# Performance work log

Hardware: AMD Instinct MI355X
Metric: run time of the kernel (lower is better)

Reference implementation:

```python
import jax, jax.numpy as jnp
import numpy as np

EMBED_DIM = 1024
NUM_HEADS = 16
HEAD_DIM = EMBED_DIM // NUM_HEADS


def setup_inputs() -> dict:
    key = jax.random.key(0)
    k_x, k_wqkv, k_bqkv, k_wp, k_bp = jax.random.split(key, 5)
    B, S = 4, 2048
    scale = 1.0 / np.sqrt(EMBED_DIM)
    return {
        "x": jax.random.normal(k_x, (B, S, EMBED_DIM), dtype=jnp.float32),
        "w_qkv": jax.random.uniform(k_wqkv, (EMBED_DIM, 3 * EMBED_DIM), jnp.float32, -scale, scale),
        "b_qkv": jax.random.uniform(k_bqkv, (3 * EMBED_DIM,), jnp.float32, -scale, scale),
        "w_proj": jax.random.uniform(k_wp, (EMBED_DIM, EMBED_DIM), jnp.float32, -scale, scale),
        "b_proj": jax.random.uniform(k_bp, (EMBED_DIM,), jnp.float32, -scale, scale),
    }


def reference(x, w_qkv, b_qkv, w_proj, b_proj):
    B, S, E = x.shape
    H, D = NUM_HEADS, HEAD_DIM
    # fused QKV projection: [B,S,3E] -> [3,B,H,S,D]
    qkv = (x @ w_qkv + b_qkv).reshape(B, S, 3, H, D).transpose(2, 0, 3, 1, 4)
    q, k, v = qkv[0], qkv[1], qkv[2]
    scores = jnp.einsum("bhqd,bhkd->bhqk", q, k) / np.sqrt(D).astype(jnp.float32)
    attn = jax.nn.softmax(scores, axis=-1)  # dropout is identity in eval
    out = jnp.einsum("bhqk,bhkd->bhqd", attn, v)
    out = out.transpose(0, 2, 1, 3).reshape(B, S, E)
    return out @ w_proj + b_proj
```

## Files before the change

kernel.cpp:

```cpp
#include <hip/hip_runtime.h>
#include <hip/hip_bf16.h>

#define PB 4
#define PS 2048
#define PH 16
#define PD 64
#define PE 1024

typedef short v8s __attribute__((ext_vector_type(8)));
typedef float v4f __attribute__((ext_vector_type(4)));

__device__ __forceinline__ ushort f2b(float f) {
  union { __hip_bfloat16 b; ushort u; } cv;
  cv.b = __float2bfloat16(f);
  return cv.u;
}

__device__ __forceinline__ void cp16(const __hip_bfloat16* g, __hip_bfloat16* l) {
  __builtin_amdgcn_global_load_lds(
      (const __attribute__((address_space(1))) void*)g,
      (__attribute__((address_space(3))) void*)l, 16, 0, 0);
}

__global__ __launch_bounds__(256) void conv_f2b(const float* __restrict__ S,
                                                __hip_bfloat16* __restrict__ D) {
  int i = blockIdx.x * 256 + threadIdx.x;
  float4 f = reinterpret_cast<const float4*>(S)[i];
  union { ushort u[4]; uint2 v; } pk;
  pk.u[0] = f2b(f.x); pk.u[1] = f2b(f.y); pk.u[2] = f2b(f.z); pk.u[3] = f2b(f.w);
  reinterpret_cast<uint2*>(D)[i] = pk.v;
}

__global__ __launch_bounds__(256) void transp_f2b(const float* __restrict__ S,
                                                  __hip_bfloat16* __restrict__ D,
                                                  int R, int C) {
  __shared__ float tile[32][33];
  const int t = threadIdx.x;
  const int tx = t & 31, ty = t >> 5;
  const int r0 = blockIdx.y * 32, c0 = blockIdx.x * 32;
#pragma unroll
  for (int i = 0; i < 4; ++i)
    tile[ty + 8 * i][tx] = S[(size_t)(r0 + ty + 8 * i) * C + c0 + tx];
  __syncthreads();
#pragma unroll
  for (int i = 0; i < 4; ++i)
    D[(size_t)(c0 + ty + 8 * i) * R + r0 + tx] = __float2bfloat16(tile[tx][ty + 8 * i]);
}

template <int MODE>
__global__ __launch_bounds__(256) void gemm_bt(
    const __hip_bfloat16* __restrict__ A, const __hip_bfloat16* __restrict__ BT,
    const float* __restrict__ bias, void* __restrict__ outv) {
  __shared__ __hip_bfloat16 As[128 * 64];
  __shared__ __hip_bfloat16 Bs[128 * 64];
  const int t = threadIdx.x;
  const int lane = t & 63, w = t >> 6;
  const int ln = lane & 15, qd = lane >> 4;
  const int wm = w >> 1, wn = w & 1;
  const int m0 = blockIdx.y * 128, n0 = blockIdx.x * 128;
  v4f acc[4][4] = {};

  for (int k0 = 0; k0 < PE; k0 += 64) {
    __syncthreads();
#pragma unroll
    for (int i = 0; i < 4; ++i) {
      int idx = t + 256 * i;
      int r = idx >> 3, cs = idx & 7;
      int cg = cs ^ (r & 7);
      cp16(A + (size_t)(m0 + r) * PE + k0 + cg * 8, As + idx * 8);
      cp16(BT + (size_t)(n0 + r) * PE + k0 + cg * 8, Bs + idx * 8);
    }
    __syncthreads();
#pragma unroll
    for (int kk = 0; kk < 2; ++kk) {
      v8s af[4], bf[4];
#pragma unroll
      for (int mb = 0; mb < 4; ++mb) {
        int ra = wm * 64 + mb * 16 + ln;
        int ca = (kk * 4 + qd) ^ (ra & 7);
        af[mb] = *reinterpret_cast<const v8s*>(As + ra * 64 + ca * 8);
      }
#pragma unroll
      for (int nb = 0; nb < 4; ++nb) {
        int rb = wn * 64 + nb * 16 + ln;
        int cb = (kk * 4 + qd) ^ (rb & 7);
        bf[nb] = *reinterpret_cast<const v8s*>(Bs + rb * 64 + cb * 8);
      }
#pragma unroll
      for (int mb = 0; mb < 4; ++mb)
#pragma unroll
        for (int nb = 0; nb < 4; ++nb)
          acc[mb][nb] = __builtin_amdgcn_mfma_f32_16x16x32_bf16(af[mb], bf[nb],
                                                                acc[mb][nb], 0, 0, 0);
    }
  }

  const int mwb = m0 + wm * 64 + qd * 4;
  const int nwb = n0 + wn * 64 + ln;
  if (MODE == 0) {
    __hip_bfloat16* QKV = (__hip_bfloat16*)outv;
#pragma unroll
    for (int nb = 0; nb < 4; ++nb) {
      int n = nwb + nb * 16;
      float bv = bias[n];
      int which = n >> 10, h = (n >> 6) & 15, d = n & 63;
#pragma unroll
      for (int mb = 0; mb < 4; ++mb) {
        int r0 = mwb + mb * 16;
        int b = r0 >> 11, s0 = r0 & (PS - 1);
        v4f a = acc[mb][nb];
        if (which == 2) {
          union { ushort u[4]; uint2 v; } pk;
#pragma unroll
          for (int i = 0; i < 4; ++i) pk.u[i] = f2b(a[i] + bv);
          size_t idx = (((size_t)(2 * PB + b) * PH + h) * PD + d) * PS + s0;
          *reinterpret_cast<uint2*>(&QKV[idx]) = pk.v;
        } else {
          float sc = (which == 0) ? 0.125f : 1.0f;
          size_t base = (((size_t)(which * PB + b) * PH + h) * PS + s0) * PD + d;
#pragma unroll
          for (int i = 0; i < 4; ++i)
            QKV[base + (size_t)i * PD] = __float2bfloat16((a[i] + bv) * sc);
        }
      }
    }
  } else {
    float* Co = (float*)outv;
#pragma unroll
    for (int nb = 0; nb < 4; ++nb) {
      int n = nwb + nb * 16;
      float bv = bias[n];
#pragma unroll
      for (int mb = 0; mb < 4; ++mb) {
        int r0 = mwb + mb * 16;
        v4f a = acc[mb][nb];
#pragma unroll
        for (int i = 0; i < 4; ++i)
          Co[(size_t)(r0 + i) * PE + n] = a[i] + bv;
      }
    }
  }
}

__global__ __launch_bounds__(256) void attn_mfma3(
    const __hip_bfloat16* __restrict__ QKV, __hip_bfloat16* __restrict__ O) {
  __shared__ __hip_bfloat16 Ks[128 * 64];
  __shared__ __hip_bfloat16 Vts[64 * 128];
  __shared__ __hip_bfloat16 Ps[128][136];
  const int t = threadIdx.x;
  const int lane = t & 63, w = t >> 6;
  const int ln = lane & 15, qd = lane >> 4;
  const int b = blockIdx.y >> 4, h = blockIdx.y & 15;
  const int q0 = blockIdx.x * 128;
  const __hip_bfloat16* Qb = QKV + (size_t)(b * PH + h) * PS * PD;
  const __hip_bfloat16* Kb = QKV + (size_t)((PB + b) * PH + h) * PS * PD;
  const __hip_bfloat16* Vb = QKV + (size_t)((2 * PB + b) * PH + h) * PD * PS;

  v8s qf[2][2];
#pragma unroll
  for (int u = 0; u < 2; ++u) {
    size_t qr = (size_t)(q0 + 32 * w + 16 * u + ln) * PD;
    qf[u][0] = *reinterpret_cast<const v8s*>(Qb + qr + qd * 8);
    qf[u][1] = *reinterpret_cast<const v8s*>(Qb + qr + 32 + qd * 8);
  }
  v4f oacc[2][4] = {};
  float lrow[2] = {0.f, 0.f};

  for (int kt = 0; kt < PS; kt += 128) {
    __syncthreads();
#pragma unroll
    for (int i = 0; i < 4; ++i) {
      int idx = t + 256 * i;
      int rk = idx >> 3, ck = (idx & 7) ^ (rk & 7);
      cp16(Kb + (size_t)(kt + rk) * PD + ck * 8, Ks + idx * 8);
      int rv = idx >> 4, cv = (idx & 15) ^ (rv & 7);
      cp16(Vb + (size_t)rv * PS + kt + cv * 8, Vts + idx * 8);
    }
    __syncthreads();

#pragma unroll
    for (int u = 0; u < 2; ++u) {
      float psum = 0.f;
#pragma unroll
      for (int nb = 0; nb < 8; ++nb) {
        int nr = nb * 16 + ln;
        int c0 = qd ^ (nr & 7);
        v8s k0 = *reinterpret_cast<const v8s*>(Ks + nr * 64 + c0 * 8);
        v8s k1 = *reinterpret_cast<const v8s*>(Ks + nr * 64 + (c0 ^ 4) * 8);
        v4f z = {};
        z = __builtin_amdgcn_mfma_f32_16x16x32_bf16(k0, qf[u][0], z, 0, 0, 0);
        v4f sv = __builtin_amdgcn_mfma_f32_16x16x32_bf16(k1, qf[u][1], z, 0, 0, 0);
        union { ushort pu[4]; uint2 pv; } pk;
#pragma unroll
        for (int i = 0; i < 4; ++i) {
          float p = __expf(sv[i]);
          psum += p;
          pk.pu[i] = f2b(p);
        }
        *reinterpret_cast<uint2*>(&Ps[32 * w + 16 * u + ln][nb * 16 + qd * 4]) = pk.pv;
      }
      psum += __shfl_xor(psum, 16);
      psum += __shfl_xor(psum, 32);
      lrow[u] += psum;
    }
    v8s pf[2][4];
#pragma unroll
    for (int u = 0; u < 2; ++u)
#pragma unroll
      for (int s = 0; s < 4; ++s)
        pf[u][s] = *reinterpret_cast<const v8s*>(
            &Ps[32 * w + 16 * u + ln][s * 32 + qd * 8]);
#pragma unroll
    for (int db = 0; db < 4; ++db) {
      int rv = db * 16 + ln;
      v4f o0 = oacc[0][db], o1 = oacc[1][db];
#pragma unroll
      for (int s = 0; s < 4; ++s) {
        int cv = (s * 4 + qd) ^ (rv & 7);
        v8s vf = *reinterpret_cast<const v8s*>(Vts + rv * 128 + cv * 8);
        o0 = __builtin_amdgcn_mfma_f32_16x16x32_bf16(pf[0][s], vf, o0, 0, 0, 0);
        o1 = __builtin_amdgcn_mfma_f32_16x16x32_bf16(pf[1][s], vf, o1, 0, 0, 0);
      }
      oacc[0][db] = o0;
      oacc[1][db] = o1;
    }
  }
#pragma unroll
  for (int u = 0; u < 2; ++u) {
#pragma unroll
    for (int i = 0; i < 4; ++i) {
      float inv = 1.f / __shfl(lrow[u], qd * 4 + i);
      int sg = q0 + 32 * w + 16 * u + qd * 4 + i;
      size_t base = (((size_t)b * PS + sg) * PH + h) * PD;
#pragma unroll
      for (int db = 0; db < 4; ++db)
        O[base + db * 16 + ln] = __float2bfloat16(oacc[u][db][i] * inv);
    }
  }
}

__device__ __forceinline__ uint2 load4bf(const float* p) {
  const float4 f = *reinterpret_cast<const float4*>(p);
  union { ushort u[4]; uint2 v; } pk;
  pk.u[0] = f2b(f.x); pk.u[1] = f2b(f.y); pk.u[2] = f2b(f.z); pk.u[3] = f2b(f.w);
  return pk.v;
}
__device__ __forceinline__ uint2 load4bf(const __hip_bfloat16* p) {
  return *reinterpret_cast<const uint2*>(p);
}

template <typename AT, int MODE>
__global__ __launch_bounds__(256) void gemm128(
    const AT* __restrict__ A, const float* __restrict__ Bm,
    const float* __restrict__ bias, void* __restrict__ outv, int ldb) {
  __shared__ __hip_bfloat16 As[128][40];
  __shared__ __hip_bfloat16 Bs[128][40];
  const int t = threadIdx.x;
  const int lane = t & 63, w = t >> 6;
  const int ln = lane & 15, qd = lane >> 4;
  const int wm = w >> 1, wn = w & 1;
  const int m0 = blockIdx.y * 128, n0 = blockIdx.x * 128;
  v4f acc[4][4] = {};
  for (int k0 = 0; k0 < PE; k0 += 32) {
    __syncthreads();
#pragma unroll
    for (int i = 0; i < 4; ++i) {
      int p = t + 256 * i;
      int m = p >> 3, kc = p & 7;
      *reinterpret_cast<uint2*>(&As[m][kc * 4]) =
          load4bf(A + (size_t)(m0 + m) * PE + k0 + kc * 4);
    }
#pragma unroll
    for (int i = 0; i < 4; ++i) {
      int p = t + 256 * i;
      int n = p & 127, kc = p >> 7;
      union { ushort u[4]; uint2 v; } pk;
#pragma unroll
      for (int r = 0; r < 4; ++r)
        pk.u[r] = f2b(Bm[(size_t)(k0 + kc * 4 + r) * ldb + n0 + n]);
      *reinterpret_cast<uint2*>(&Bs[n][kc * 4]) = pk.v;
    }
    __syncthreads();
    v8s af[4], bf[4];
#pragma unroll
    for (int mb = 0; mb < 4; ++mb)
      af[mb] = *reinterpret_cast<const v8s*>(&As[wm * 64 + mb * 16 + ln][qd * 8]);
#pragma unroll
    for (int nb = 0; nb < 4; ++nb)
      bf[nb] = *reinterpret_cast<const v8s*>(&Bs[wn * 64 + nb * 16 + ln][qd * 8]);
#pragma unroll
    for (int mb = 0; mb < 4; ++mb)
#pragma unroll
      for (int nb = 0; nb < 4; ++nb)
        acc[mb][nb] = __builtin_amdgcn_mfma_f32_16x16x32_bf16(af[mb], bf[nb],
                                                              acc[mb][nb], 0, 0, 0);
  }
  const int mwb = m0 + wm * 64 + qd * 4;
  const int nwb = n0 + wn * 64 + ln;
  if (MODE == 0) {
    __hip_bfloat16* QKV = (__hip_bfloat16*)outv;
#pragma unroll
    for (int nb = 0; nb < 4; ++nb) {
      int n = nwb + nb * 16;
      float bv = bias[n];
      int which = n >> 10, h = (n >> 6) & 15, d = n & 63;
#pragma unroll
      for (int mb = 0; mb < 4; ++mb) {
        int r0 = mwb + mb * 16;
        int b = r0 >> 11, s0 = r0 & (PS - 1);
        v4f a = acc[mb][nb];
        if (which == 2) {
          union { ushort u[4]; uint2 v; } pk;
#pragma unroll
          for (int i = 0; i < 4; ++i) pk.u[i] = f2b(a[i] + bv);
          size_t idx = (((size_t)(2 * PB + b) * PH + h) * PD + d) * PS + s0;
          *reinterpret_cast<uint2*>(&QKV[idx]) = pk.v;
        } else {
          float sc = (which == 0) ? 0.125f : 1.0f;
          size_t base = (((size_t)(which * PB + b) * PH + h) * PS + s0) * PD + d;
#pragma unroll
          for (int i = 0; i < 4; ++i)
            QKV[base + (size_t)i * PD] = __float2bfloat16((a[i] + bv) * sc);
        }
      }
    }
  } else {
    float* Co = (float*)outv;
#pragma unroll
    for (int nb = 0; nb < 4; ++nb) {
      int n = nwb + nb * 16;
      float bv = bias[n];
#pragma unroll
      for (int mb = 0; mb < 4; ++mb) {
        int r0 = mwb + mb * 16;
        v4f a = acc[mb][nb];
#pragma unroll
        for (int i = 0; i < 4; ++i)
          Co[(size_t)(r0 + i) * PE + n] = a[i] + bv;
      }
    }
  }
}

extern "C" void kernel_launch(void* const* d_in, const int* in_sizes, int n_in,
                              void* d_out, int out_size, void* d_ws,
                              size_t ws_size, hipStream_t stream) {
  const float* x = (const float*)d_in[0];
  const float* w_qkv = (const float*)d_in[1];
  const float* b_qkv = (const float*)d_in[2];
  const float* w_proj = (const float*)d_in[3];
  const float* b_proj = (const float*)d_in[4];
  float* out = (float*)d_out;

  const size_t xE = (size_t)PB * PS * PE;
  const size_t wqE = (size_t)PE * 3 * PE;
  const size_t wpE = (size_t)PE * PE;
  const size_t qkvE = (size_t)3 * PB * PH * PS * PD;
  const size_t needMain = (xE + wqE + wpE + qkvE) * 2;

  dim3 blk(256);
  dim3 gq(24, 64), ga(16, 64), gp(8, 64);

  if (ws_size >= needMain) {
    __hip_bfloat16* xb = (__hip_bfloat16*)d_ws;
    __hip_bfloat16* wqkvT = xb + xE;
    __hip_bfloat16* wprojT = wqkvT + wqE;
    __hip_bfloat16* qkv = wprojT + wpE;
    __hip_bfloat16* o = xb;

    conv_f2b<<<dim3(xE / 1024), blk, 0, stream>>>(x, xb);
    transp_f2b<<<dim3(96, 32), blk, 0, stream>>>(w_qkv, wqkvT, PE, 3 * PE);
    transp_f2b<<<dim3(32, 32), blk, 0, stream>>>(w_proj, wprojT, PE, PE);
    gemm_bt<0><<<gq, blk, 0, stream>>>(xb, wqkvT, b_qkv, qkv);
    attn_mfma3<<<ga, blk, 0, stream>>>(qkv, o);
    gemm_bt<1><<<gp, blk, 0, stream>>>(o, wprojT, b_proj, out);
  } else {
    __hip_bfloat16* qkv = (__hip_bfloat16*)d_ws;
    if (ws_size >= (qkvE + xE) * 2) {
      __hip_bfloat16* o = qkv + qkvE;
      gemm128<float, 0><<<gq, blk, 0, stream>>>(x, w_qkv, b_qkv, qkv, 3 * PE);
      attn_mfma3<<<ga, blk, 0, stream>>>(qkv, o);
      gemm128<__hip_bfloat16, 1><<<gp, blk, 0, stream>>>(o, w_proj, b_proj, out, PE);
    } else {
      __hip_bfloat16* o = (__hip_bfloat16*)d_out;
      float* tmp = (float*)d_ws;
      gemm128<float, 0><<<gq, blk, 0, stream>>>(x, w_qkv, b_qkv, qkv, 3 * PE);
      attn_mfma3<<<ga, blk, 0, stream>>>(qkv, o);
      gemm128<__hip_bfloat16, 1><<<gp, blk, 0, stream>>>(o, w_proj, b_proj, tmp, PE);
      hipMemcpyAsync(d_out, tmp, xE * sizeof(float), hipMemcpyDeviceToDevice, stream);
    }
  }
}
```

Before: 310.3 us.

## Enlarge GEMM tile to 256x128 and hoist K fragments in attention

The bf16 GEMM block tile grows from 128x128 to 256x128. Each of the four waves now owns a 64x128 sub-tile with 32 accumulators, which halves the grid in M and raises arithmetic intensity per shared-memory load of B. In the attention kernel, K fragments are loaded from LDS once per tile into registers and reused by both query sub-blocks, instead of being reloaded per sub-block. Both changes raise register pressure, which may reduce occupancy or cause spills. The larger LDS footprint for A and the smaller grid (768 and 256 blocks) could hurt latency hiding.

```diff
diff --git a/kernel.cpp b/kernel.cpp
--- a/kernel.cpp
+++ b/kernel.cpp
@@ -51,56 +51,61 @@
 __global__ __launch_bounds__(256) void gemm_bt(
     const __hip_bfloat16* __restrict__ A, const __hip_bfloat16* __restrict__ BT,
     const float* __restrict__ bias, void* __restrict__ outv) {
-  __shared__ __hip_bfloat16 As[128 * 64];
+  __shared__ __hip_bfloat16 As[256 * 64];
   __shared__ __hip_bfloat16 Bs[128 * 64];
   const int t = threadIdx.x;
   const int lane = t & 63, w = t >> 6;
   const int ln = lane & 15, qd = lane >> 4;
-  const int wm = w >> 1, wn = w & 1;
-  const int m0 = blockIdx.y * 128, n0 = blockIdx.x * 128;
-  v4f acc[4][4] = {};
+  const int m0 = blockIdx.y * 256, n0 = blockIdx.x * 128;
+  v4f acc[4][8] = {};
 
   for (int k0 = 0; k0 < PE; k0 += 64) {
     __syncthreads();
+#pragma unroll
+    for (int i = 0; i < 8; ++i) {
+      int idx = t + 256 * i;
+      int r = idx >> 3, cs = idx & 7;
+      int cg = cs ^ (r & 7);
+      cp16(A + (size_t)(m0 + r) * PE + k0 + cg * 8, As + idx * 8);
+    }
 #pragma unroll
     for (int i = 0; i < 4; ++i) {
       int idx = t + 256 * i;
       int r = idx >> 3, cs = idx & 7;
       int cg = cs ^ (r & 7);
-      cp16(A + (size_t)(m0 + r) * PE + k0 + cg * 8, As + idx * 8);
       cp16(BT + (size_t)(n0 + r) * PE + k0 + cg * 8, Bs + idx * 8);
     }
     __syncthreads();
 #pragma unroll
     for (int kk = 0; kk < 2; ++kk) {
-      v8s af[4], bf[4];
+      v8s af[4], bf[8];
 #pragma unroll
       for (int mb = 0; mb < 4; ++mb) {
-        int ra = wm * 64 + mb * 16 + ln;
+        int ra = w * 64 + mb * 16 + ln;
         int ca = (kk * 4 + qd) ^ (ra & 7);
         af[mb] = *reinterpret_cast<const v8s*>(As + ra * 64 + ca * 8);
       }
 #pragma unroll
-      for (int nb = 0; nb < 4; ++nb) {
-        int rb = wn * 64 + nb * 16 + ln;
+      for (int nb = 0; nb < 8; ++nb) {
+        int rb = nb * 16 + ln;
         int cb = (kk * 4 + qd) ^ (rb & 7);
         bf[nb] = *reinterpret_cast<const v8s*>(Bs + rb * 64 + cb * 8);
       }
 #pragma unroll
       for (int mb = 0; mb < 4; ++mb)
 #pragma unroll
-        for (int nb = 0; nb < 4; ++nb)
+        for (int nb = 0; nb < 8; ++nb)
           acc[mb][nb] = __builtin_amdgcn_mfma_f32_16x16x32_bf16(af[mb], bf[nb],
                                                                 acc[mb][nb], 0, 0, 0);
     }
   }
 
-  const int mwb = m0 + wm * 64 + qd * 4;
-  const int nwb = n0 + wn * 64 + ln;
+  const int mwb = m0 + w * 64 + qd * 4;
+  const int nwb = n0 + ln;
   if (MODE == 0) {
     __hip_bfloat16* QKV = (__hip_bfloat16*)outv;
 #pragma unroll
-    for (int nb = 0; nb < 4; ++nb) {
+    for (int nb = 0; nb < 8; ++nb) {
       int n = nwb + nb * 16;
       float bv = bias[n];
       int which = n >> 10, h = (n >> 6) & 15, d = n & 63;
@@ -127,7 +132,7 @@
   } else {
     float* Co = (float*)outv;
 #pragma unroll
-    for (int nb = 0; nb < 4; ++nb) {
+    for (int nb = 0; nb < 8; ++nb) {
       int n = nwb + nb * 16;
       float bv = bias[n];
 #pragma unroll
@@ -178,18 +183,22 @@
     }
     __syncthreads();
 
+    v8s kf[8][2];
+#pragma unroll
+    for (int nb = 0; nb < 8; ++nb) {
+      int nr = nb * 16 + ln;
+      int c0 = qd ^ (nr & 7);
+      kf[nb][0] = *reinterpret_cast<const v8s*>(Ks + nr * 64 + c0 * 8);
+      kf[nb][1] = *reinterpret_cast<const v8s*>(Ks + nr * 64 + (c0 ^ 4) * 8);
+    }
 #pragma unroll
     for (int u = 0; u < 2; ++u) {
       float psum = 0.f;
 #pragma unroll
       for (int nb = 0; nb < 8; ++nb) {
-        int nr = nb * 16 + ln;
-        int c0 = qd ^ (nr & 7);
-        v8s k0 = *reinterpret_cast<const v8s*>(Ks + nr * 64 + c0 * 8);
-        v8s k1 = *reinterpret_cast<const v8s*>(Ks + nr * 64 + (c0 ^ 4) * 8);
         v4f z = {};
-        z = __builtin_amdgcn_mfma_f32_16x16x32_bf16(k0, qf[u][0], z, 0, 0, 0);
-        v4f sv = __builtin_amdgcn_mfma_f32_16x16x32_bf16(k1, qf[u][1], z, 0, 0, 0);
+        z = __builtin_amdgcn_mfma_f32_16x16x32_bf16(kf[nb][0], qf[u][0], z, 0, 0, 0);
+        v4f sv = __builtin_amdgcn_mfma_f32_16x16x32_bf16(kf[nb][1], qf[u][1], z, 0, 0, 0);
         union { ushort pu[4]; uint2 pv; } pk;
 #pragma unroll
         for (int i = 0; i < 4; ++i) {
@@ -359,7 +368,7 @@
   const size_t needMain = (xE + wqE + wpE + qkvE) * 2;
 
   dim3 blk(256);
-  dim3 gq(24, 64), ga(16, 64), gp(8, 64);
+  dim3 gq(24, 32), ga(16, 64), gp(8, 32);
 
   if (ws_size >= needMain) {
     __hip_bfloat16* xb = (__hip_bfloat16*)d_ws;
@@ -376,17 +385,18 @@
     gemm_bt<1><<<gp, blk, 0, stream>>>(o, wprojT, b_proj, out);
   } else {
     __hip_bfloat16* qkv = (__hip_bfloat16*)d_ws;
+    dim3 gq128(24, 64), gp128(8, 64);
     if (ws_size >= (qkvE + xE) * 2) {
       __hip_bfloat16* o = qkv + qkvE;
-      gemm128<float, 0><<<gq, blk, 0, stream>>>(x, w_qkv, b_qkv, qkv, 3 * PE);
+      gemm128<float, 0><<<gq128, blk, 0, stream>>>(x, w_qkv, b_qkv, qkv, 3 * PE);
       attn_mfma3<<<ga, blk, 0, stream>>>(qkv, o);
-      gemm128<__hip_bfloat16, 1><<<gp, blk, 0, stream>>>(o, w_proj, b_proj, out, PE);
+      gemm128<__hip_bfloat16, 1><<<gp128, blk, 0, stream>>>(o, w_proj, b_proj, out, PE);
     } else {
       __hip_bfloat16* o = (__hip_bfloat16*)d_out;
       float* tmp = (float*)d_ws;
-      gemm128<float, 0><<<gq, blk, 0, stream>>>(x, w_qkv, b_qkv, qkv, 3 * PE);
+      gemm128<float, 0><<<gq128, blk, 0, stream>>>(x, w_qkv, b_qkv, qkv, 3 * PE);
       attn_mfma3<<<ga, blk, 0, stream>>>(qkv, o);
-      gemm128<__hip_bfloat16, 1><<<gp, blk, 0, stream>>>(o, w_proj, b_proj, tmp, PE);
+      gemm128<__hip_bfloat16, 1><<<gp128, blk, 0, stream>>>(o, w_proj, b_proj, tmp, PE);
       hipMemcpyAsync(d_out, tmp, xE * sizeof(float), hipMemcpyDeviceToDevice, stream);
     }
   }
```

After: 338.6 us. 1.09x slower.

## Read V directly from global, per-wave swizzled P buffer, exp2 softmax

Applied to the files above, without the earlier changes.

The attention kernel stops staging V tiles in shared memory and reads V fragments straight from global memory (through cache). It also replaces the shared 128x136 P buffer with per-wave swizzled 16x128 buffers, and hoists the K fragment loads out of the u-loop into registers. Q is prescaled by log2(e)/8 so exp2f can replace __expf. These changes aim to cut LDS traffic, shared-memory footprint and the exp cost, at the price of uncoalesced global V reads and higher register pressure. The softmax still has no max subtraction, which was already the case before.

```diff
diff --git a/kernel.cpp b/kernel.cpp
--- a/kernel.cpp
+++ b/kernel.cpp
@@ -1,11 +1,14 @@
 #include <hip/hip_runtime.h>
 #include <hip/hip_bf16.h>
+#include <math.h>
 
 #define PB 4
 #define PS 2048
 #define PH 16
 #define PD 64
 #define PE 1024
+
+#define QSCALE 0.1803368801111244f
 
 typedef short v8s __attribute__((ext_vector_type(8)));
 typedef float v4f __attribute__((ext_vector_type(4)));
@@ -116,7 +119,7 @@
           size_t idx = (((size_t)(2 * PB + b) * PH + h) * PD + d) * PS + s0;
           *reinterpret_cast<uint2*>(&QKV[idx]) = pk.v;
         } else {
-          float sc = (which == 0) ? 0.125f : 1.0f;
+          float sc = (which == 0) ? QSCALE : 1.0f;
           size_t base = (((size_t)(which * PB + b) * PH + h) * PS + s0) * PD + d;
 #pragma unroll
           for (int i = 0; i < 4; ++i)
@@ -142,11 +145,10 @@
   }
 }
 
-__global__ __launch_bounds__(256) void attn_mfma3(
+__global__ __launch_bounds__(256) void attn_mfma4(
     const __hip_bfloat16* __restrict__ QKV, __hip_bfloat16* __restrict__ O) {
   __shared__ __hip_bfloat16 Ks[128 * 64];
-  __shared__ __hip_bfloat16 Vts[64 * 128];
-  __shared__ __hip_bfloat16 Ps[128][136];
+  __shared__ __hip_bfloat16 Psr[4][16 * 128];
   const int t = threadIdx.x;
   const int lane = t & 63, w = t >> 6;
   const int ln = lane & 15, qd = lane >> 4;
@@ -155,6 +157,7 @@
   const __hip_bfloat16* Qb = QKV + (size_t)(b * PH + h) * PS * PD;
   const __hip_bfloat16* Kb = QKV + (size_t)((PB + b) * PH + h) * PS * PD;
   const __hip_bfloat16* Vb = QKV + (size_t)((2 * PB + b) * PH + h) * PD * PS;
+  __hip_bfloat16* myP = &Psr[w][0];
 
   v8s qf[2][2];
 #pragma unroll
@@ -173,51 +176,52 @@
       int idx = t + 256 * i;
       int rk = idx >> 3, ck = (idx & 7) ^ (rk & 7);
       cp16(Kb + (size_t)(kt + rk) * PD + ck * 8, Ks + idx * 8);
-      int rv = idx >> 4, cv = (idx & 15) ^ (rv & 7);
-      cp16(Vb + (size_t)rv * PS + kt + cv * 8, Vts + idx * 8);
-    }
-    __syncthreads();
-
+    }
+    __syncthreads();
+
+    v8s kf[8][2];
+#pragma unroll
+    for (int nb = 0; nb < 8; ++nb) {
+      int nr = nb * 16 + ln;
+      int c0 = qd ^ (nr & 7);
+      kf[nb][0] = *reinterpret_cast<const v8s*>(Ks + nr * 64 + c0 * 8);
+      kf[nb][1] = *reinterpret_cast<const v8s*>(Ks + nr * 64 + (c0 ^ 4) * 8);
+    }
+    v8s pf[2][4];
 #pragma unroll
     for (int u = 0; u < 2; ++u) {
       float psum = 0.f;
 #pragma unroll
       for (int nb = 0; nb < 8; ++nb) {
-        int nr = nb * 16 + ln;
-        int c0 = qd ^ (nr & 7);
-        v8s k0 = *reinterpret_cast<const v8s*>(Ks + nr * 64 + c0 * 8);
-        v8s k1 = *reinterpret_cast<const v8s*>(Ks + nr * 64 + (c0 ^ 4) * 8);
         v4f z = {};
-        z = __builtin_amdgcn_mfma_f32_16x16x32_bf16(k0, qf[u][0], z, 0, 0, 0);
-        v4f sv = __builtin_amdgcn_mfma_f32_16x16x32_bf16(k1, qf[u][1], z, 0, 0, 0);
+        z = __builtin_amdgcn_mfma_f32_16x16x32_bf16(kf[nb][0], qf[u][0], z, 0, 0, 0);
+        v4f sv = __builtin_amdgcn_mfma_f32_16x16x32_bf16(kf[nb][1], qf[u][1], z, 0, 0, 0);
         union { ushort pu[4]; uint2 pv; } pk;
 #pragma unroll
         for (int i = 0; i < 4; ++i) {
-          float p = __expf(sv[i]);
+          float p = exp2f(sv[i]);
           psum += p;
           pk.pu[i] = f2b(p);
         }
-        *reinterpret_cast<uint2*>(&Ps[32 * w + 16 * u + ln][nb * 16 + qd * 4]) = pk.pv;
+        int cst = (nb * 2 + (qd >> 1)) ^ (ln & 7);
+        *reinterpret_cast<uint2*>(myP + ln * 128 + cst * 8 + (qd & 1) * 4) = pk.pv;
       }
       psum += __shfl_xor(psum, 16);
       psum += __shfl_xor(psum, 32);
       lrow[u] += psum;
-    }
-    v8s pf[2][4];
-#pragma unroll
-    for (int u = 0; u < 2; ++u)
-#pragma unroll
-      for (int s = 0; s < 4; ++s)
-        pf[u][s] = *reinterpret_cast<const v8s*>(
-            &Ps[32 * w + 16 * u + ln][s * 32 + qd * 8]);
+#pragma unroll
+      for (int s = 0; s < 4; ++s) {
+        int crd = (s * 4 + qd) ^ (ln & 7);
+        pf[u][s] = *reinterpret_cast<const v8s*>(myP + ln * 128 + crd * 8);
+      }
+    }
 #pragma unroll
     for (int db = 0; db < 4; ++db) {
-      int rv = db * 16 + ln;
+      const __hip_bfloat16* vrow = Vb + (size_t)(db * 16 + ln) * PS + kt;
       v4f o0 = oacc[0][db], o1 = oacc[1][db];
 #pragma unroll
       for (int s = 0; s < 4; ++s) {
-        int cv = (s * 4 + qd) ^ (rv & 7);
-        v8s vf = *reinterpret_cast<const v8s*>(Vts + rv * 128 + cv * 8);
+        v8s vf = *reinterpret_cast<const v8s*>(vrow + s * 32 + qd * 8);
         o0 = __builtin_amdgcn_mfma_f32_16x16x32_bf16(pf[0][s], vf, o0, 0, 0, 0);
         o1 = __builtin_amdgcn_mfma_f32_16x16x32_bf16(pf[1][s], vf, o1, 0, 0, 0);
       }
@@ -316,7 +320,7 @@
           size_t idx = (((size_t)(2 * PB + b) * PH + h) * PD + d) * PS + s0;
           *reinterpret_cast<uint2*>(&QKV[idx]) = pk.v;
         } else {
-          float sc = (which == 0) ? 0.125f : 1.0f;
+          float sc = (which == 0) ? QSCALE : 1.0f;
           size_t base = (((size_t)(which * PB + b) * PH + h) * PS + s0) * PD + d;
 #pragma unroll
           for (int i = 0; i < 4; ++i)
@@ -372,21 +376,22 @@
     transp_f2b<<<dim3(96, 32), blk, 0, stream>>>(w_qkv, wqkvT, PE, 3 * PE);
     transp_f2b<<<dim3(32, 32), blk, 0, stream>>>(w_proj, wprojT, PE, PE);
     gemm_bt<0><<<gq, blk, 0, stream>>>(xb, wqkvT, b_qkv, qkv);
-    attn_mfma3<<<ga, blk, 0, stream>>>(qkv, o);
+    attn_mfma4<<<ga, blk, 0, stream>>>(qkv, o);
     gemm_bt<1><<<gp, blk, 0, stream>>>(o, wprojT, b_proj, out);
   } else {
     __hip_bfloat16* qkv = (__hip_bfloat16*)d_ws;
+    dim3 gq128(24, 64), gp128(8, 64);
     if (ws_size >= (qkvE + xE) * 2) {
       __hip_bfloat16* o = qkv + qkvE;
-      gemm128<float, 0><<<gq, blk, 0, stream>>>(x, w_qkv, b_qkv, qkv, 3 * PE);
-      attn_mfma3<<<ga, blk, 0, stream>>>(qkv, o);
-      gemm128<__hip_bfloat16, 1><<<gp, blk, 0, stream>>>(o, w_proj, b_proj, out, PE);
+      gemm128<float, 0><<<gq128, blk, 0, stream>>>(x, w_qkv, b_qkv, qkv, 3 * PE);
+      attn_mfma4<<<ga, blk, 0, stream>>>(qkv, o);
+      gemm128<__hip_bfloat16, 1><<<gp128, blk, 0, stream>>>(o, w_proj, b_proj, out, PE);
     } else {
       __hip_bfloat16* o = (__hip_bfloat16*)d_out;
       float* tmp = (float*)d_ws;
-      gemm128<float, 0><<<gq, blk, 0, stream>>>(x, w_qkv, b_qkv, qkv, 3 * PE);
-      attn_mfma3<<<ga, blk, 0, stream>>>(qkv, o);
-      gemm128<__hip_bfloat16, 1><<<gp, blk, 0, stream>>>(o, w_proj, b_proj, tmp, PE);
+      gemm128<float, 0><<<gq128, blk, 0, stream>>>(x, w_qkv, b_qkv, qkv, 3 * PE);
+      attn_mfma4<<<ga, blk, 0, stream>>>(qkv, o);
+      gemm128<__hip_bfloat16, 1><<<gp128, blk, 0, stream>>>(o, w_proj, b_proj, tmp, PE);
       hipMemcpyAsync(d_out, tmp, xE * sizeof(float), hipMemcpyDeviceToDevice, stream);
     }
   }
```

New measurement: 365.1 us. 17.7% more time.
